# Kernel tuning notes

Measured on AMD Instinct MI355X. Metric: run time of the kernel, lower is better.

The kernel has to match this reference:

```python
import jax, jax.numpy as jnp
import numpy as np

IN_DIM = 128
OUT_DIM = 128


def setup_inputs() -> dict:
    key = jax.random.key(0)
    k1, k2, k3, k4, k5, k6 = jax.random.split(key, 6)
    B, N, F, K = 4, 20000, IN_DIM, 16
    x = jax.random.normal(k1, (B, N, F), dtype=jnp.float32)
    adj = jax.random.randint(k2, (B, N, K), 0, N, dtype=jnp.int64)
    lim = 1.0 / np.sqrt(IN_DIM)
    W_self = jax.random.uniform(k3, (IN_DIM, OUT_DIM), jnp.float32, -lim, lim)
    b_self = jax.random.uniform(k4, (OUT_DIM,), jnp.float32, -lim, lim)
    W_nei = jax.random.uniform(k5, (IN_DIM, OUT_DIM), jnp.float32, -lim, lim)
    b_nei = jax.random.uniform(k6, (OUT_DIM,), jnp.float32, -lim, lim)
    return {"x": x, "adj": adj, "W_self": W_self, "b_self": b_self,
            "W_nei": W_nei, "b_nei": b_nei}


def reference(x, adj, W_self, b_self, W_nei, b_nei):
    # x: [B,N,F], adj: [B,N,K] indices into N
    # gather neighbor features per batch: [B,N,K,F]
    nei = jax.vmap(lambda xb, ab: xb[ab])(x, adj)
    nei_feat = nei.mean(axis=2)  # [B,N,F]
    out = jnp.einsum('bnf,fo->bno', x, W_self) + b_self \
        + jnp.einsum('bnf,fo->bno', nei_feat, W_nei) + b_nei
    return jax.nn.relu(out)
```

## Files before the change

kernel.cpp:

```cpp
#include <hip/hip_runtime.h>
#include <hip/hip_bf16.h>

#define NBATCH 4
#define NNODE  20000
#define NF     128
#define NK     16
#define NROWS  (NBATCH * NNODE)
#define NBLK_G 1250
#define NBLK_F 5000
#define WTF_BYTES 65536
#define BIAS_OFF  WTF_BYTES
#define S_OFF     (WTF_BYTES + 1024)
#define Y_OFF     (S_OFF + NROWS * NF * 2)

typedef __attribute__((ext_vector_type(8))) short bf16x8_t;
typedef __attribute__((ext_vector_type(4))) float f32x4_t;
typedef __attribute__((ext_vector_type(2))) float f32x2_t;

__device__ __forceinline__ unsigned int f2bf(float f) {
  unsigned int u = __float_as_uint(f);
  u += 0x7fffu + ((u >> 16) & 1u);
  return u >> 16;
}

__device__ __forceinline__ int xcd_swz_g(int orig) {
  const int xcd = orig & 7, i = orig >> 3;
  const int q = NBLK_G / 8, r = NBLK_G % 8;
  return (xcd < r ? xcd * (q + 1) : r * (q + 1) + (xcd - r) * q) + i;
}

__device__ __forceinline__ int xcd_swz_f(int orig) {
  return (orig & 7) * (NBLK_F / 8) + (orig >> 3);
}

__device__ __forceinline__ void stage16(const void* g, void* l) {
  __builtin_amdgcn_global_load_lds(
      (const __attribute__((address_space(1))) unsigned int*)g,
      (__attribute__((address_space(3))) unsigned int*)l, 16, 0, 0);
}

__global__ __launch_bounds__(256) void sage_wprep(
    const float* __restrict__ Ws, const float* __restrict__ bs,
    const float* __restrict__ Wn, const float* __restrict__ bn,
    unsigned char* __restrict__ ws)
{
  const int bid = blockIdx.x, tid = threadIdx.x;
  if (bid == 16) {
    if (tid < NF) ((float*)(ws + BIAS_OFF))[tid] = bs[tid] + bn[tid];
    return;
  }
  const int ft = bid * 256 + tid;
  const int gc = ft >> 8;
  const int s  = (ft >> 6) & 3;
  const int l  = ft & 63;
  const int colg = gc * 16 + (l & 15);
  const int k0 = s * 32 + ((l >> 4) << 3);
  const float* W = (colg < NF) ? Ws : Wn;
  const int col = (colg < NF) ? colg : colg - NF;
  unsigned int w[4];
#pragma unroll
  for (int jj = 0; jj < 4; ++jj) {
    const float va = W[(k0 + 2 * jj) * NF + col];
    const float vb = W[(k0 + 2 * jj + 1) * NF + col];
    w[jj] = f2bf(va) | (f2bf(vb) << 16);
  }
  *reinterpret_cast<uint4*>(ws + (size_t)ft * 16) = make_uint4(w[0], w[1], w[2], w[3]);
}

__global__ __launch_bounds__(256) void sage_gemm(
    const float* __restrict__ x, unsigned char* __restrict__ ws)
{
  __shared__ __align__(16) unsigned char sW[32768];
  const int tid = threadIdx.x, lane = tid & 63, wid = tid >> 6;
  const int bid = xcd_swz_g(blockIdx.x);
  const int fl = lane & 15, q = lane >> 4;
  const int myrow = bid * 64 + wid * 16 + fl;

  const float* xr = x + (size_t)myrow * NF + q * 8;
  float4 xv[8];
#pragma unroll
  for (int s = 0; s < 4; ++s) {
    xv[2 * s]     = *reinterpret_cast<const float4*>(xr + s * 32);
    xv[2 * s + 1] = *reinterpret_cast<const float4*>(xr + s * 32 + 4);
  }
#pragma unroll
  for (int i = 0; i < 8; ++i) {
    const int c0 = i * 256 + wid * 64;
    stage16(ws + (size_t)(c0 + lane) * 16, sW + (size_t)c0 * 16);
  }
  __builtin_amdgcn_sched_barrier(0);

  bf16x8_t bx[4];
#pragma unroll
  for (int s = 0; s < 4; ++s) {
    union { unsigned int u[4]; bf16x8_t v; } r;
    r.u[0] = f2bf(xv[2 * s].x) | (f2bf(xv[2 * s].y) << 16);
    r.u[1] = f2bf(xv[2 * s].z) | (f2bf(xv[2 * s].w) << 16);
    r.u[2] = f2bf(xv[2 * s + 1].x) | (f2bf(xv[2 * s + 1].y) << 16);
    r.u[3] = f2bf(xv[2 * s + 1].z) | (f2bf(xv[2 * s + 1].w) << 16);
    bx[s] = r.v;
  }
  __syncthreads();

  const bf16x8_t* sWf = reinterpret_cast<const bf16x8_t*>(sW);

  f32x4_t acc[8];
#pragma unroll
  for (int t = 0; t < 8; ++t) acc[t] = (f32x4_t){0.f, 0.f, 0.f, 0.f};
#pragma unroll
  for (int t = 0; t < 8; ++t)
#pragma unroll
    for (int s = 0; s < 4; ++s)
      acc[t] = __builtin_amdgcn_mfma_f32_16x16x32_bf16(
          sWf[(t * 4 + s) * 64 + lane], bx[s], acc[t], 0, 0, 0);

  const float* bias = reinterpret_cast<const float*>(ws + BIAS_OFF);
  unsigned short* sp = reinterpret_cast<unsigned short*>(ws + S_OFF);
#pragma unroll
  for (int t = 0; t < 8; ++t) {
    const int c4 = t * 16 + q * 4;
    const float4 b = *reinterpret_cast<const float4*>(bias + c4);
    uint2 p;
    p.x = f2bf(acc[t][0] + b.x) | (f2bf(acc[t][1] + b.y) << 16);
    p.y = f2bf(acc[t][2] + b.z) | (f2bf(acc[t][3] + b.w) << 16);
    *reinterpret_cast<uint2*>(sp + (size_t)myrow * NF + c4) = p;
  }

  __syncthreads();
#pragma unroll
  for (int i = 0; i < 8; ++i) {
    const int c0 = i * 256 + wid * 64;
    stage16(ws + 32768 + (size_t)(c0 + lane) * 16, sW + (size_t)c0 * 16);
  }
  __syncthreads();

#pragma unroll
  for (int t = 0; t < 8; ++t) acc[t] = (f32x4_t){0.f, 0.f, 0.f, 0.f};
#pragma unroll
  for (int t = 0; t < 8; ++t)
#pragma unroll
    for (int s = 0; s < 4; ++s)
      acc[t] = __builtin_amdgcn_mfma_f32_16x16x32_bf16(
          sWf[(t * 4 + s) * 64 + lane], bx[s], acc[t], 0, 0, 0);

  unsigned char* yp = ws + Y_OFF;
#pragma unroll
  for (int t = 0; t < 8; ++t) {
    const int c4 = t * 16 + q * 4;
    int w8 = __builtin_amdgcn_cvt_pk_fp8_f32(acc[t][0], acc[t][1], 0, false);
    w8 = __builtin_amdgcn_cvt_pk_fp8_f32(acc[t][2], acc[t][3], w8, true);
    *reinterpret_cast<unsigned int*>(yp + (size_t)myrow * NF + c4) =
        (unsigned int)w8;
  }
}

__global__ __launch_bounds__(256) void sage_fin(
    const unsigned char* __restrict__ ws, const int* __restrict__ adj,
    float* __restrict__ out)
{
  const int tid = threadIdx.x, lane = tid & 63, wid = tid >> 6;
  const int bid = xcd_swz_f(blockIdx.x);
  const int rg = lane >> 4, fl = lane & 15;
  const int row = bid * 16 + wid * 4 + rg;
  const int b = row / NNODE;

  const unsigned short* sp = reinterpret_cast<const unsigned short*>(ws + S_OFF);
  const unsigned char* yb = ws + Y_OFF + (size_t)b * NNODE * NF + fl * 8;

  const int4* a4 = reinterpret_cast<const int4*>(adj + (size_t)row * NK);
  const int4 t0 = a4[0], t1 = a4[1], t2 = a4[2], t3 = a4[3];
  const int idx[16] = {t0.x, t0.y, t0.z, t0.w, t1.x, t1.y, t1.z, t1.w,
                       t2.x, t2.y, t2.z, t2.w, t3.x, t3.y, t3.z, t3.w};

  const uint4 sv = *reinterpret_cast<const uint4*>(sp + (size_t)row * NF + fl * 8);

  uint2 v[16];
#pragma unroll
  for (int k = 0; k < 16; ++k)
    v[k] = *reinterpret_cast<const uint2*>(yb + (size_t)idx[k] * NF);
  __builtin_amdgcn_sched_barrier(0);

  f32x2_t g0 = {0.f, 0.f}, g1 = {0.f, 0.f}, g2 = {0.f, 0.f}, g3 = {0.f, 0.f};
#pragma unroll
  for (int k = 0; k < 16; ++k) {
    g0 += __builtin_amdgcn_cvt_pk_f32_fp8(v[k].x, false);
    g1 += __builtin_amdgcn_cvt_pk_f32_fp8(v[k].x, true);
    g2 += __builtin_amdgcn_cvt_pk_f32_fp8(v[k].y, false);
    g3 += __builtin_amdgcn_cvt_pk_f32_fp8(v[k].y, true);
  }

  float se[8];
  se[0] = __uint_as_float(sv.x << 16); se[1] = __uint_as_float(sv.x & 0xffff0000u);
  se[2] = __uint_as_float(sv.y << 16); se[3] = __uint_as_float(sv.y & 0xffff0000u);
  se[4] = __uint_as_float(sv.z << 16); se[5] = __uint_as_float(sv.z & 0xffff0000u);
  se[6] = __uint_as_float(sv.w << 16); se[7] = __uint_as_float(sv.w & 0xffff0000u);

  const float sc = 1.f / 16.f;
  float4 o0, o1;
  o0.x = fmaxf(se[0] + g0[0] * sc, 0.f);
  o0.y = fmaxf(se[1] + g0[1] * sc, 0.f);
  o0.z = fmaxf(se[2] + g1[0] * sc, 0.f);
  o0.w = fmaxf(se[3] + g1[1] * sc, 0.f);
  o1.x = fmaxf(se[4] + g2[0] * sc, 0.f);
  o1.y = fmaxf(se[5] + g2[1] * sc, 0.f);
  o1.z = fmaxf(se[6] + g3[0] * sc, 0.f);
  o1.w = fmaxf(se[7] + g3[1] * sc, 0.f);
  float* op = out + (size_t)row * NF + fl * 8;
  *reinterpret_cast<float4*>(op)     = o0;
  *reinterpret_cast<float4*>(op + 4) = o1;
}

extern "C" void kernel_launch(void* const* d_in, const int* in_sizes, int n_in,
                              void* d_out, int out_size, void* d_ws, size_t ws_size,
                              hipStream_t stream) {
  const float* x     = (const float*)d_in[0];
  const int*   adj   = (const int*)d_in[1];
  const float* Wself = (const float*)d_in[2];
  const float* bself = (const float*)d_in[3];
  const float* Wnei  = (const float*)d_in[4];
  const float* bnei  = (const float*)d_in[5];
  float* out = (float*)d_out;
  unsigned char* ws = (unsigned char*)d_ws;

  hipLaunchKernelGGL(sage_wprep, dim3(17), dim3(256), 0, stream,
                     Wself, bself, Wnei, bnei, ws);
  hipLaunchKernelGGL(sage_gemm, dim3(NBLK_G), dim3(256), 0, stream, x, ws);
  hipLaunchKernelGGL(sage_fin, dim3(NBLK_F), dim3(256), 0, stream,
                     ws, adj, out);
}
```

Before: 52.22 us.

## Split GEMM output columns across waves with register-resident weights, dropping LDS staging

The GEMM kernel used to give each wave 16 rows and all 256 output columns (self and neighbour), staging weights through LDS in two phases with barriers. Now each block handles 16 rows and each wave owns 64 output columns, loading its weight fragments directly from global/L2 into registers. There is no shared memory or __syncthreads, and the block count rises 4x. This removes LDS staging and barriers and may raise occupancy, but every block re-reads x rows across 4 waves and the weight slice per block, adding L2 traffic.

Result: slower. 64.92 us (+24.3%).

```diff
diff --git a/kernel.cpp b/kernel.cpp
--- a/kernel.cpp
+++ b/kernel.cpp
@@ -6,7 +6,7 @@
 #define NF     128
 #define NK     16
 #define NROWS  (NBATCH * NNODE)
-#define NBLK_G 1250
+#define NBLK_G 5000
 #define NBLK_F 5000
 #define WTF_BYTES 65536
 #define BIAS_OFF  WTF_BYTES
@@ -23,20 +23,8 @@
   return u >> 16;
 }
 
-__device__ __forceinline__ int xcd_swz_g(int orig) {
-  const int xcd = orig & 7, i = orig >> 3;
-  const int q = NBLK_G / 8, r = NBLK_G % 8;
-  return (xcd < r ? xcd * (q + 1) : r * (q + 1) + (xcd - r) * q) + i;
-}
-
-__device__ __forceinline__ int xcd_swz_f(int orig) {
-  return (orig & 7) * (NBLK_F / 8) + (orig >> 3);
-}
-
-__device__ __forceinline__ void stage16(const void* g, void* l) {
-  __builtin_amdgcn_global_load_lds(
-      (const __attribute__((address_space(1))) unsigned int*)g,
-      (__attribute__((address_space(3))) unsigned int*)l, 16, 0, 0);
+__device__ __forceinline__ int xcd_swz8(int orig, int nblk) {
+  return (orig & 7) * (nblk >> 3) + (orig >> 3);
 }
 
 __global__ __launch_bounds__(256) void sage_wprep(
@@ -67,26 +55,38 @@
   *reinterpret_cast<uint4*>(ws + (size_t)ft * 16) = make_uint4(w[0], w[1], w[2], w[3]);
 }
 
-__global__ __launch_bounds__(256) void sage_gemm(
+__global__ __launch_bounds__(256, 3) void sage_gemm(
     const float* __restrict__ x, unsigned char* __restrict__ ws)
 {
-  __shared__ __align__(16) unsigned char sW[32768];
   const int tid = threadIdx.x, lane = tid & 63, wid = tid >> 6;
-  const int bid = xcd_swz_g(blockIdx.x);
+  const int bid = xcd_swz8(blockIdx.x, NBLK_G);
   const int fl = lane & 15, q = lane >> 4;
-  const int myrow = bid * 64 + wid * 16 + fl;
-
-  const float* xr = x + (size_t)myrow * NF + q * 8;
+  const int myrow = bid * 16 + fl;
+
+  const bf16x8_t* wtf = reinterpret_cast<const bf16x8_t*>(ws);
+  const float* bias = reinterpret_cast<const float*>(ws + BIAS_OFF);
+
+  bf16x8_t wf[16];
+#pragma unroll
+  for (int t4 = 0; t4 < 4; ++t4)
+#pragma unroll
+    for (int s = 0; s < 4; ++s)
+      wf[t4 * 4 + s] = wtf[((wid * 4 + t4) * 4 + s) * 64 + lane];
+
+  const float* xr = x + (size_t)myrow * NF;
   float4 xv[8];
 #pragma unroll
   for (int s = 0; s < 4; ++s) {
-    xv[2 * s]     = *reinterpret_cast<const float4*>(xr + s * 32);
-    xv[2 * s + 1] = *reinterpret_cast<const float4*>(xr + s * 32 + 4);
-  }
-#pragma unroll
-  for (int i = 0; i < 8; ++i) {
-    const int c0 = i * 256 + wid * 64;
-    stage16(ws + (size_t)(c0 + lane) * 16, sW + (size_t)c0 * 16);
+    xv[2 * s]     = *reinterpret_cast<const float4*>(xr + s * 32 + q * 8);
+    xv[2 * s + 1] = *reinterpret_cast<const float4*>(xr + s * 32 + q * 8 + 4);
+  }
+
+  float4 bv[4] = {};
+  if (wid < 2) {
+#pragma unroll
+    for (int t4 = 0; t4 < 4; ++t4)
+      bv[t4] = *reinterpret_cast<const float4*>(
+          bias + (wid * 4 + t4) * 16 + q * 4);
   }
   __builtin_amdgcn_sched_barrier(0);
 
@@ -100,57 +100,37 @@
     r.u[3] = f2bf(xv[2 * s + 1].z) | (f2bf(xv[2 * s + 1].w) << 16);
     bx[s] = r.v;
   }
-  __syncthreads();
-
-  const bf16x8_t* sWf = reinterpret_cast<const bf16x8_t*>(sW);
-
-  f32x4_t acc[8];
-#pragma unroll
-  for (int t = 0; t < 8; ++t) acc[t] = (f32x4_t){0.f, 0.f, 0.f, 0.f};
-#pragma unroll
-  for (int t = 0; t < 8; ++t)
+
+  f32x4_t acc[4];
+#pragma unroll
+  for (int t4 = 0; t4 < 4; ++t4) acc[t4] = (f32x4_t){0.f, 0.f, 0.f, 0.f};
+#pragma unroll
+  for (int t4 = 0; t4 < 4; ++t4)
 #pragma unroll
     for (int s = 0; s < 4; ++s)
-      acc[t] = __builtin_amdgcn_mfma_f32_16x16x32_bf16(
-          sWf[(t * 4 + s) * 64 + lane], bx[s], acc[t], 0, 0, 0);
-
-  const float* bias = reinterpret_cast<const float*>(ws + BIAS_OFF);
-  unsigned short* sp = reinterpret_cast<unsigned short*>(ws + S_OFF);
-#pragma unroll
-  for (int t = 0; t < 8; ++t) {
-    const int c4 = t * 16 + q * 4;
-    const float4 b = *reinterpret_cast<const float4*>(bias + c4);
-    uint2 p;
-    p.x = f2bf(acc[t][0] + b.x) | (f2bf(acc[t][1] + b.y) << 16);
-    p.y = f2bf(acc[t][2] + b.z) | (f2bf(acc[t][3] + b.w) << 16);
-    *reinterpret_cast<uint2*>(sp + (size_t)myrow * NF + c4) = p;
-  }
-
-  __syncthreads();
-#pragma unroll
-  for (int i = 0; i < 8; ++i) {
-    const int c0 = i * 256 + wid * 64;
-    stage16(ws + 32768 + (size_t)(c0 + lane) * 16, sW + (size_t)c0 * 16);
-  }
-  __syncthreads();
-
-#pragma unroll
-  for (int t = 0; t < 8; ++t) acc[t] = (f32x4_t){0.f, 0.f, 0.f, 0.f};
-#pragma unroll
-  for (int t = 0; t < 8; ++t)
-#pragma unroll
-    for (int s = 0; s < 4; ++s)
-      acc[t] = __builtin_amdgcn_mfma_f32_16x16x32_bf16(
-          sWf[(t * 4 + s) * 64 + lane], bx[s], acc[t], 0, 0, 0);
-
-  unsigned char* yp = ws + Y_OFF;
-#pragma unroll
-  for (int t = 0; t < 8; ++t) {
-    const int c4 = t * 16 + q * 4;
-    int w8 = __builtin_amdgcn_cvt_pk_fp8_f32(acc[t][0], acc[t][1], 0, false);
-    w8 = __builtin_amdgcn_cvt_pk_fp8_f32(acc[t][2], acc[t][3], w8, true);
-    *reinterpret_cast<unsigned int*>(yp + (size_t)myrow * NF + c4) =
-        (unsigned int)w8;
+      acc[t4] = __builtin_amdgcn_mfma_f32_16x16x32_bf16(
+          wf[t4 * 4 + s], bx[s], acc[t4], 0, 0, 0);
+
+  if (wid < 2) {
+    unsigned short* sp = reinterpret_cast<unsigned short*>(ws + S_OFF);
+#pragma unroll
+    for (int t4 = 0; t4 < 4; ++t4) {
+      const int c4 = (wid * 4 + t4) * 16 + q * 4;
+      uint2 p;
+      p.x = f2bf(acc[t4][0] + bv[t4].x) | (f2bf(acc[t4][1] + bv[t4].y) << 16);
+      p.y = f2bf(acc[t4][2] + bv[t4].z) | (f2bf(acc[t4][3] + bv[t4].w) << 16);
+      *reinterpret_cast<uint2*>(sp + (size_t)myrow * NF + c4) = p;
+    }
+  } else {
+    unsigned char* yp = ws + Y_OFF;
+#pragma unroll
+    for (int t4 = 0; t4 < 4; ++t4) {
+      const int c4 = ((wid - 2) * 4 + t4) * 16 + q * 4;
+      int w8 = __builtin_amdgcn_cvt_pk_fp8_f32(acc[t4][0], acc[t4][1], 0, false);
+      w8 = __builtin_amdgcn_cvt_pk_fp8_f32(acc[t4][2], acc[t4][3], w8, true);
+      *reinterpret_cast<unsigned int*>(yp + (size_t)myrow * NF + c4) =
+          (unsigned int)w8;
+    }
   }
 }
 
@@ -159,7 +139,7 @@
     float* __restrict__ out)
 {
   const int tid = threadIdx.x, lane = tid & 63, wid = tid >> 6;
-  const int bid = xcd_swz_f(blockIdx.x);
+  const int bid = xcd_swz8(blockIdx.x, NBLK_F);
   const int rg = lane >> 4, fl = lane & 15;
   const int row = bid * 16 + wid * 4 + rg;
   const int b = row / NNODE;
```

## Stage full weight matrix at once and load x coalesced via swizzled LDS

Applied to the files above, without the earlier changes.

The GEMM kernel now stages both weight halves (64KB) into LDS in one pass instead of two sequential 32KB passes with extra barriers. It computes all 16 output tiles in a single MFMA loop. x is loaded with fully coalesced row-contiguous float4 reads, converted to bf16, and written to an XOR-swizzled LDS tile before being read back in MFMA operand layout. This removes a mid-kernel barrier and stage, at the cost of about 80KB LDS per block, which lowers occupancy, and twice as many live accumulators.

Result: no change. 52.59 us (+0.7%).

```diff
diff --git a/kernel.cpp b/kernel.cpp
--- a/kernel.cpp
+++ b/kernel.cpp
@@ -39,6 +39,10 @@
       (__attribute__((address_space(3))) unsigned int*)l, 16, 0, 0);
 }
 
+__device__ __forceinline__ int swzx(int row, int kbyte) {
+  return (row << 8) + (kbyte ^ ((row & 15) << 4));
+}
+
 __global__ __launch_bounds__(256) void sage_wprep(
     const float* __restrict__ Ws, const float* __restrict__ bs,
     const float* __restrict__ Wn, const float* __restrict__ bn,
@@ -70,51 +74,56 @@
 __global__ __launch_bounds__(256) void sage_gemm(
     const float* __restrict__ x, unsigned char* __restrict__ ws)
 {
-  __shared__ __align__(16) unsigned char sW[32768];
+  __shared__ __align__(16) unsigned char sW[65536];
+  __shared__ __align__(16) unsigned char sX[16384];
+
   const int tid = threadIdx.x, lane = tid & 63, wid = tid >> 6;
   const int bid = xcd_swz_g(blockIdx.x);
+  const int row0 = bid * 64;
   const int fl = lane & 15, q = lane >> 4;
-  const int myrow = bid * 64 + wid * 16 + fl;
-
-  const float* xr = x + (size_t)myrow * NF + q * 8;
+
   float4 xv[8];
 #pragma unroll
-  for (int s = 0; s < 4; ++s) {
-    xv[2 * s]     = *reinterpret_cast<const float4*>(xr + s * 32);
-    xv[2 * s + 1] = *reinterpret_cast<const float4*>(xr + s * 32 + 4);
-  }
-#pragma unroll
-  for (int i = 0; i < 8; ++i) {
+  for (int j = 0; j < 8; ++j) {
+    const int c = j * 256 + tid;
+    const int r = c >> 5, f4 = c & 31;
+    xv[j] = *reinterpret_cast<const float4*>(x + (size_t)(row0 + r) * NF + f4 * 4);
+  }
+#pragma unroll
+  for (int i = 0; i < 16; ++i) {
     const int c0 = i * 256 + wid * 64;
     stage16(ws + (size_t)(c0 + lane) * 16, sW + (size_t)c0 * 16);
   }
-  __builtin_amdgcn_sched_barrier(0);
+#pragma unroll
+  for (int j = 0; j < 8; ++j) {
+    const int c = j * 256 + tid;
+    const int r = c >> 5, f4 = c & 31;
+    uint2 p;
+    p.x = f2bf(xv[j].x) | (f2bf(xv[j].y) << 16);
+    p.y = f2bf(xv[j].z) | (f2bf(xv[j].w) << 16);
+    *reinterpret_cast<uint2*>(sX + swzx(r, f4 * 8)) = p;
+  }
+  __syncthreads();
 
   bf16x8_t bx[4];
-#pragma unroll
-  for (int s = 0; s < 4; ++s) {
-    union { unsigned int u[4]; bf16x8_t v; } r;
-    r.u[0] = f2bf(xv[2 * s].x) | (f2bf(xv[2 * s].y) << 16);
-    r.u[1] = f2bf(xv[2 * s].z) | (f2bf(xv[2 * s].w) << 16);
-    r.u[2] = f2bf(xv[2 * s + 1].x) | (f2bf(xv[2 * s + 1].y) << 16);
-    r.u[3] = f2bf(xv[2 * s + 1].z) | (f2bf(xv[2 * s + 1].w) << 16);
-    bx[s] = r.v;
-  }
-  __syncthreads();
-
+  const int xr = wid * 16 + fl;
+#pragma unroll
+  for (int s = 0; s < 4; ++s)
+    bx[s] = *reinterpret_cast<const bf16x8_t*>(sX + swzx(xr, s * 64 + q * 16));
+
+  f32x4_t acc[16];
+#pragma unroll
+  for (int t = 0; t < 16; ++t) acc[t] = (f32x4_t){0.f, 0.f, 0.f, 0.f};
   const bf16x8_t* sWf = reinterpret_cast<const bf16x8_t*>(sW);
-
-  f32x4_t acc[8];
-#pragma unroll
-  for (int t = 0; t < 8; ++t) acc[t] = (f32x4_t){0.f, 0.f, 0.f, 0.f};
-#pragma unroll
-  for (int t = 0; t < 8; ++t)
+#pragma unroll
+  for (int t = 0; t < 16; ++t)
 #pragma unroll
     for (int s = 0; s < 4; ++s)
       acc[t] = __builtin_amdgcn_mfma_f32_16x16x32_bf16(
           sWf[(t * 4 + s) * 64 + lane], bx[s], acc[t], 0, 0, 0);
 
   const float* bias = reinterpret_cast<const float*>(ws + BIAS_OFF);
+  const int myrow = row0 + wid * 16 + fl;
   unsigned short* sp = reinterpret_cast<unsigned short*>(ws + S_OFF);
 #pragma unroll
   for (int t = 0; t < 8; ++t) {
@@ -125,28 +134,10 @@
     p.y = f2bf(acc[t][2] + b.z) | (f2bf(acc[t][3] + b.w) << 16);
     *reinterpret_cast<uint2*>(sp + (size_t)myrow * NF + c4) = p;
   }
-
-  __syncthreads();
-#pragma unroll
-  for (int i = 0; i < 8; ++i) {
-    const int c0 = i * 256 + wid * 64;
-    stage16(ws + 32768 + (size_t)(c0 + lane) * 16, sW + (size_t)c0 * 16);
-  }
-  __syncthreads();
-
-#pragma unroll
-  for (int t = 0; t < 8; ++t) acc[t] = (f32x4_t){0.f, 0.f, 0.f, 0.f};
-#pragma unroll
-  for (int t = 0; t < 8; ++t)
-#pragma unroll
-    for (int s = 0; s < 4; ++s)
-      acc[t] = __builtin_amdgcn_mfma_f32_16x16x32_bf16(
-          sWf[(t * 4 + s) * 64 + lane], bx[s], acc[t], 0, 0, 0);
-
   unsigned char* yp = ws + Y_OFF;
 #pragma unroll
-  for (int t = 0; t < 8; ++t) {
-    const int c4 = t * 16 + q * 4;
+  for (int t = 8; t < 16; ++t) {
+    const int c4 = (t - 8) * 16 + q * 4;
     int w8 = __builtin_amdgcn_cvt_pk_fp8_f32(acc[t][0], acc[t][1], 0, false);
     w8 = __builtin_amdgcn_cvt_pk_fp8_f32(acc[t][2], acc[t][3], w8, true);
     *reinterpret_cast<unsigned int*>(yp + (size_t)myrow * NF + c4) =
```
